# Kernel tuning notes

Hardware: AMD Instinct MI355X
Metric: run time of the kernel (lower is better)

The kernel has to match this reference:

```python
import jax, jax.numpy as jnp
import numpy as np


def color_bin(x, n_bins):
    """Per-image 3D color histogram over n_bins**3 flat bins.
    x: [B, 3, H, W] float in ~[-1, 1]. Returns [B, n_bins**3] float32.
    """
    B, C, H, W = x.shape
    n_tot = n_bins ** 3
    # torch color_bins: i*(2/n_bins) - 1 for i in 1..n_bins-1
    boundaries = jnp.arange(1, n_bins, dtype=jnp.float32) * (2.0 / n_bins) - 1.0
    # torch.bucketize(right=False) == searchsorted side='left'
    idx = jnp.searchsorted(boundaries, x.reshape(B, C, H * W), side='left')  # [B,3,HW] int
    scale = jnp.array([1, n_bins, n_bins ** 2], dtype=idx.dtype)
    flat = jnp.einsum('bcp,c->bp', idx, scale)  # [B, HW], values in [0, n_tot)
    # torch.histc(bins, n_tot, min=0, max=n_tot-1) on exact integers == bincount
    hist = jax.vmap(lambda f: jnp.bincount(f, length=n_tot))(flat)
    return hist.astype(jnp.float32) / (H * W)


def setup_inputs() -> dict:
    key = jax.random.key(0)
    k1, k2 = jax.random.split(key)
    inp = jax.random.normal(k1, (8, 3, 1024, 1024), dtype=jnp.float32)
    style = jax.random.normal(k2, (1, 3, 1024, 1024), dtype=jnp.float32)
    return {"input": inp, "style_image": style, "n_bins": 16}


def reference(input, style_image, n_bins):
    # target histogram from the style image (detached in torch; ints anyway)
    target = color_bin(style_image, n_bins).squeeze(0)  # [n_tot]
    cols = color_bin(input, n_bins)                     # [B, n_tot]
    # F.l1_loss(cols, target.repeat(B, 1)) with mean reduction
    loss = jnp.mean(jnp.abs(cols - target[None, :]))
    return loss
```

## Files before the change

### kernel.cpp

```cpp
#include <hip/hip_runtime.h>

#define HW      (1024 * 1024)
#define HW4     (HW / 4)
#define NBINS   4096
#define NIMG    9
#define BPI     64
#define THREADS 256
#define F4_PER_BLOCK (HW4 / BPI)

__device__ __forceinline__ int bin16(float x) {
    int lo = 0;
    if (0.0f < x) lo = 8;
    if ((float)(lo + 4) * 0.125f - 1.0f < x) lo += 4;
    if ((float)(lo + 2) * 0.125f - 1.0f < x) lo += 2;
    if ((float)(lo + 1) * 0.125f - 1.0f < x) lo += 1;
    return lo;
}

__device__ __forceinline__ int bin3(float r, float g, float b) {
    return bin16(r) + 16 * bin16(g) + 256 * bin16(b);
}

__global__ __launch_bounds__(THREADS) void hist_kernel(
        const float* __restrict__ input,
        const float* __restrict__ style,
        int* __restrict__ ghist) {
    __shared__ int lh[NBINS];
    const int img = blockIdx.y;
    const float* base = (img < 8) ? (input + (size_t)img * 3 * HW) : style;

    for (int i = threadIdx.x; i < NBINS; i += THREADS) lh[i] = 0;
    __syncthreads();

    const float4* c0 = (const float4*)(base);
    const float4* c1 = (const float4*)(base + HW);
    const float4* c2 = (const float4*)(base + 2 * HW);
    const int start = blockIdx.x * F4_PER_BLOCK;

    for (int j = threadIdx.x; j < F4_PER_BLOCK; j += THREADS) {
        const int p = start + j;
        float4 r = c0[p];
        float4 g = c1[p];
        float4 b = c2[p];
        atomicAdd(&lh[bin3(r.x, g.x, b.x)], 1);
        atomicAdd(&lh[bin3(r.y, g.y, b.y)], 1);
        atomicAdd(&lh[bin3(r.z, g.z, b.z)], 1);
        atomicAdd(&lh[bin3(r.w, g.w, b.w)], 1);
    }
    __syncthreads();

    int* gh = ghist + (size_t)img * NBINS;
    for (int i = threadIdx.x; i < NBINS; i += THREADS) {
        const int v = lh[i];
        if (v) atomicAdd(&gh[i], v);
    }
}

__global__ __launch_bounds__(1024) void loss_kernel(
        const int* __restrict__ ghist, float* __restrict__ out) {
    __shared__ long long part[16];
    const int* tgt = ghist + 8 * NBINS;
    long long acc = 0;
    for (int e = threadIdx.x; e < 8 * NBINS; e += 1024) {
        const int b = e >> 12;
        const int i = e & (NBINS - 1);
        const int d = ghist[b * NBINS + i] - tgt[i];
        acc += (d < 0) ? (long long)(-d) : (long long)d;
    }
    for (int off = 32; off; off >>= 1) acc += __shfl_down(acc, off, 64);
    const int lane = threadIdx.x & 63;
    const int wv   = threadIdx.x >> 6;
    if (lane == 0) part[wv] = acc;
    __syncthreads();
    if (wv == 0) {
        long long t = (lane < 16) ? part[lane] : 0;
        for (int off = 8; off; off >>= 1) t += __shfl_down(t, off, 64);
        if (lane == 0) {
            out[0] = (float)((double)t / (1048576.0 * 32768.0));
        }
    }
}

extern "C" void kernel_launch(void* const* d_in, const int* in_sizes, int n_in,
                              void* d_out, int out_size, void* d_ws, size_t ws_size,
                              hipStream_t stream) {
    const float* input = (const float*)d_in[0];
    const float* style = (const float*)d_in[1];
    int* ghist = (int*)d_ws;

    hipMemsetAsync(d_ws, 0, NIMG * NBINS * sizeof(int), stream);

    dim3 grid(BPI, NIMG);
    hipLaunchKernelGGL(hist_kernel, grid, dim3(THREADS), 0, stream,
                       input, style, ghist);
    hipLaunchKernelGGL(loss_kernel, dim3(1), dim3(1024), 0, stream,
                       ghist, (float*)d_out);
}
```

Before: 175.7 us.

## Fuse loss into histogram kernel via last-block pattern, unroll nontemporal loads

Merges the separate loss kernel into the histogram kernel. An atomic block counter lets the last block to finish compute the L1 loss, which removes one kernel launch. It also doubles blocks per image, unrolls the loop four times with nontemporal vector loads for more memory-level parallelism, and shrinks the reduction accumulators to 32-bit. The final reduction now runs on only 256 threads in a single block, and the counter adds a fence per block.

```diff
diff --git a/kernel.cpp b/kernel.cpp
--- a/kernel.cpp
+++ b/kernel.cpp
@@ -4,9 +4,12 @@
 #define HW4     (HW / 4)
 #define NBINS   4096
 #define NIMG    9
-#define BPI     64
+#define BPI     128
 #define THREADS 256
 #define F4_PER_BLOCK (HW4 / BPI)
+#define NBLOCKS (NIMG * BPI)
+
+typedef float f4 __attribute__((ext_vector_type(4)));
 
 __device__ __forceinline__ int bin16(float x) {
     int lo = 0;
@@ -21,31 +24,51 @@
     return bin16(r) + 16 * bin16(g) + 256 * bin16(b);
 }
 
-__global__ __launch_bounds__(THREADS) void hist_kernel(
+__device__ __forceinline__ void acc4(int* lh, f4 r, f4 g, f4 b) {
+    atomicAdd(&lh[bin3(r.x, g.x, b.x)], 1);
+    atomicAdd(&lh[bin3(r.y, g.y, b.y)], 1);
+    atomicAdd(&lh[bin3(r.z, g.z, b.z)], 1);
+    atomicAdd(&lh[bin3(r.w, g.w, b.w)], 1);
+}
+
+__global__ __launch_bounds__(THREADS) void hist_loss_kernel(
         const float* __restrict__ input,
         const float* __restrict__ style,
-        int* __restrict__ ghist) {
+        int* __restrict__ ghist,
+        int* __restrict__ ctr,
+        float* __restrict__ out) {
     __shared__ int lh[NBINS];
+    __shared__ int last_flag;
     const int img = blockIdx.y;
+    const int blk = blockIdx.x;
     const float* base = (img < 8) ? (input + (size_t)img * 3 * HW) : style;
 
     for (int i = threadIdx.x; i < NBINS; i += THREADS) lh[i] = 0;
     __syncthreads();
 
-    const float4* c0 = (const float4*)(base);
-    const float4* c1 = (const float4*)(base + HW);
-    const float4* c2 = (const float4*)(base + 2 * HW);
-    const int start = blockIdx.x * F4_PER_BLOCK;
+    const f4* c0 = (const f4*)(base);
+    const f4* c1 = (const f4*)(base + HW);
+    const f4* c2 = (const f4*)(base + 2 * HW);
+    const int start = blk * F4_PER_BLOCK;
 
-    for (int j = threadIdx.x; j < F4_PER_BLOCK; j += THREADS) {
-        const int p = start + j;
-        float4 r = c0[p];
-        float4 g = c1[p];
-        float4 b = c2[p];
-        atomicAdd(&lh[bin3(r.x, g.x, b.x)], 1);
-        atomicAdd(&lh[bin3(r.y, g.y, b.y)], 1);
-        atomicAdd(&lh[bin3(r.z, g.z, b.z)], 1);
-        atomicAdd(&lh[bin3(r.w, g.w, b.w)], 1);
+    for (int j = threadIdx.x; j < F4_PER_BLOCK; j += 4 * THREADS) {
+        const int p0 = start + j;
+        f4 r0 = __builtin_nontemporal_load(&c0[p0]);
+        f4 r1 = __builtin_nontemporal_load(&c0[p0 + THREADS]);
+        f4 r2 = __builtin_nontemporal_load(&c0[p0 + 2 * THREADS]);
+        f4 r3 = __builtin_nontemporal_load(&c0[p0 + 3 * THREADS]);
+        f4 g0 = __builtin_nontemporal_load(&c1[p0]);
+        f4 g1 = __builtin_nontemporal_load(&c1[p0 + THREADS]);
+        f4 g2 = __builtin_nontemporal_load(&c1[p0 + 2 * THREADS]);
+        f4 g3 = __builtin_nontemporal_load(&c1[p0 + 3 * THREADS]);
+        f4 b0 = __builtin_nontemporal_load(&c2[p0]);
+        f4 b1 = __builtin_nontemporal_load(&c2[p0 + THREADS]);
+        f4 b2 = __builtin_nontemporal_load(&c2[p0 + 2 * THREADS]);
+        f4 b3 = __builtin_nontemporal_load(&c2[p0 + 3 * THREADS]);
+        acc4(lh, r0, g0, b0);
+        acc4(lh, r1, g1, b1);
+        acc4(lh, r2, g2, b2);
+        acc4(lh, r3, g3, b3);
     }
     __syncthreads();
 
@@ -54,30 +77,43 @@
         const int v = lh[i];
         if (v) atomicAdd(&gh[i], v);
     }
-}
 
-__global__ __launch_bounds__(1024) void loss_kernel(
-        const int* __restrict__ ghist, float* __restrict__ out) {
-    __shared__ long long part[16];
-    const int* tgt = ghist + 8 * NBINS;
-    long long acc = 0;
-    for (int e = threadIdx.x; e < 8 * NBINS; e += 1024) {
+    __syncthreads();
+    if (threadIdx.x == 0) {
+        __threadfence();
+        const int prev = __hip_atomic_fetch_add(ctr, 1, __ATOMIC_ACQ_REL,
+                                                __HIP_MEMORY_SCOPE_AGENT);
+        last_flag = (prev == NBLOCKS - 1);
+    }
+    __syncthreads();
+    if (!last_flag) return;
+
+    __threadfence();
+
+    for (int i = threadIdx.x; i < NBINS; i += THREADS)
+        lh[i] = __hip_atomic_load(&ghist[8 * NBINS + i], __ATOMIC_RELAXED,
+                                  __HIP_MEMORY_SCOPE_AGENT);
+    __syncthreads();
+
+    int acc = 0;
+    for (int e = threadIdx.x; e < 8 * NBINS; e += THREADS) {
         const int b = e >> 12;
         const int i = e & (NBINS - 1);
-        const int d = ghist[b * NBINS + i] - tgt[i];
-        acc += (d < 0) ? (long long)(-d) : (long long)d;
+        const int c = __hip_atomic_load(&ghist[b * NBINS + i], __ATOMIC_RELAXED,
+                                        __HIP_MEMORY_SCOPE_AGENT);
+        const int d = c - lh[i];
+        acc += (d < 0) ? -d : d;
     }
     for (int off = 32; off; off >>= 1) acc += __shfl_down(acc, off, 64);
+    __shared__ int partsum[4];
     const int lane = threadIdx.x & 63;
     const int wv   = threadIdx.x >> 6;
-    if (lane == 0) part[wv] = acc;
+    if (lane == 0) partsum[wv] = acc;
     __syncthreads();
-    if (wv == 0) {
-        long long t = (lane < 16) ? part[lane] : 0;
-        for (int off = 8; off; off >>= 1) t += __shfl_down(t, off, 64);
-        if (lane == 0) {
-            out[0] = (float)((double)t / (1048576.0 * 32768.0));
-        }
+    if (threadIdx.x == 0) {
+        const long long t = (long long)partsum[0] + partsum[1]
+                          + (long long)partsum[2] + partsum[3];
+        out[0] = (float)((double)t / 34359738368.0);
     }
 }
 
@@ -87,12 +123,10 @@
     const float* input = (const float*)d_in[0];
     const float* style = (const float*)d_in[1];
     int* ghist = (int*)d_ws;
+    int* ctr   = ghist + NIMG * NBINS;
 
-    hipMemsetAsync(d_ws, 0, NIMG * NBINS * sizeof(int), stream);
+    hipMemsetAsync(d_ws, 0, (NIMG * NBINS + 1) * sizeof(int), stream);
 
-    dim3 grid(BPI, NIMG);
-    hipLaunchKernelGGL(hist_kernel, grid, dim3(THREADS), 0, stream,
-                       input, style, ghist);
-    hipLaunchKernelGGL(loss_kernel, dim3(1), dim3(1024), 0, stream,
-                       ghist, (float*)d_out);
+    hipLaunchKernelGGL(hist_loss_kernel, dim3(BPI, NIMG), dim3(THREADS), 0,
+                       stream, input, style, ghist, ctr, (float*)d_out);
 }
```

New measurement: 278.5 us. 58.5% more time.
